# Optimization experiments

Measured on AMD Instinct MI355X. Metric: run time of the kernel, lower is better.

## Reference

```python
import jax, jax.numpy as jnp
import numpy as np
import math

N_HEAD = 16
D_MODEL = 1024
KSIZE = 3
PAD = 1


def _conv1d(x, w, b, pad):
    # x: [B, C_in, S], w: [C_out, C_in, K] (torch Conv1d layout)
    y = jax.lax.conv_general_dilated(
        x, w, window_strides=(1,), padding=[(pad, pad)],
        dimension_numbers=("NCH", "OIH", "NCH"))
    return y + b[None, :, None]


def setup_inputs() -> dict:
    key = jax.random.key(0)
    ks = jax.random.split(key, 10)
    B, S, D = 2, 2048, D_MODEL
    sc = 1.0 / math.sqrt(D)
    return {
        "q": jax.random.normal(ks[0], (B, S, D), jnp.float32),
        "k": jax.random.normal(ks[1], (B, S, D), jnp.float32),
        "v": jax.random.normal(ks[2], (B, S, D), jnp.float32),
        "wq_w": jax.random.normal(ks[3], (D, D, KSIZE), jnp.float32) * sc,
        "wq_b": jnp.zeros((D,), jnp.float32),
        "wk_w": jax.random.normal(ks[4], (D, D, KSIZE), jnp.float32) * sc,
        "wk_b": jnp.zeros((D,), jnp.float32),
        "wv_w": jax.random.normal(ks[5], (D, D, 1), jnp.float32) * sc,
        "wv_b": jnp.zeros((D,), jnp.float32),
        "wc_w": jax.random.normal(ks[6], (D, D), jnp.float32) * sc,
        "wc_b": jnp.zeros((D,), jnp.float32),
    }


def reference(q, k, v, wq_w, wq_b, wk_w, wk_b, wv_w, wv_b, wc_w, wc_b):
    B, S, D = q.shape
    h = N_HEAD
    d = D // h
    # channels-first for conv projections: [B, D, S]
    qc = _conv1d(jnp.swapaxes(q, 1, 2), wq_w, wq_b, PAD)
    kc = _conv1d(jnp.swapaxes(k, 1, 2), wk_w, wk_b, PAD)
    vc = _conv1d(jnp.swapaxes(v, 1, 2), wv_w, wv_b, 0)
    # faithful to torch: view(b, d, h, s) then transpose(1,2).transpose(2,3) -> [b, h, s, d]
    # (head index is the FAST axis of the channel dim, matching the original)
    qh = jnp.transpose(qc.reshape(B, d, h, S), (0, 2, 3, 1))
    kh = jnp.transpose(kc.reshape(B, d, h, S), (0, 2, 3, 1))
    vh = jnp.transpose(vc.reshape(B, d, h, S), (0, 2, 3, 1))
    scores = jnp.einsum("bhqd,bhkd->bhqk", qh, kh) / math.sqrt(d)
    attn = jax.nn.softmax(scores, axis=-1)
    out = jnp.einsum("bhqk,bhkd->bhqd", attn, vh)
    # concat: [b,h,s,d] -> [b,s,h*d]
    out = jnp.transpose(out, (0, 2, 1, 3)).reshape(B, S, D)
    # torch Linear: x @ W^T + b
    return out @ wc_w.T + wc_b
```

## Files before the change

### kernel.cpp

```cpp
#include <hip/hip_runtime.h>
#include <hip/hip_bf16.h>

#define SS 2048
#define DDIM 1024

typedef unsigned short u16;
typedef unsigned int u32;
typedef __attribute__((ext_vector_type(8))) short bf16x8_t;
typedef __attribute__((ext_vector_type(4))) float f32x4_t;

__device__ __forceinline__ u16 f2bf(float f) {
  __hip_bfloat16 h = __float2bfloat16(f);
  return *reinterpret_cast<u16*>(&h);
}

__device__ __forceinline__ void gld16(const void* g, void* lds_base) {
  __builtin_amdgcn_global_load_lds(
      (const __attribute__((address_space(1))) u32*)(uintptr_t)g,
      (__attribute__((address_space(3))) u32*)(u32)(uintptr_t)lds_base,
      16, 0, 0);
}

__global__ void zero_kernel(u32* zb) { zb[threadIdx.x] = 0u; }

__global__ __launch_bounds__(256) void convert3_kernel(
    const float* __restrict__ q, const float* __restrict__ k,
    const float* __restrict__ v, u16* __restrict__ Xq, u16* __restrict__ Xk,
    u16* __restrict__ Xv) {
  const int z = blockIdx.y;
  const float* src = (z == 0) ? q : (z == 1) ? k : v;
  u16* dst = (z == 0) ? Xq : (z == 1) ? Xk : Xv;
  int i = blockIdx.x * 256 + threadIdx.x;
  const float4* s = (const float4*)src + (size_t)i * 2;
  float4 f0 = s[0], f1 = s[1];
  u16 o[8] = {f2bf(f0.x), f2bf(f0.y), f2bf(f0.z), f2bf(f0.w),
              f2bf(f1.x), f2bf(f1.y), f2bf(f1.z), f2bf(f1.w)};
  *(uint4*)(dst + (size_t)i * 8) = *(const uint4*)o;
}

__global__ __launch_bounds__(256) void repack3_kernel(
    const float* __restrict__ wq, const float* __restrict__ wk,
    u16* __restrict__ Wqr, u16* __restrict__ Wkr) {
  const float* w = blockIdx.y ? wk : wq;
  u16* out = blockIdx.y ? Wkr : Wqr;
  int o = blockIdx.x;
  for (int j = threadIdx.x; j < 3072; j += 256) {
    int i = j / 3, t = j - i * 3;
    out[(size_t)o * 3072 + t * 1024 + i] = f2bf(w[(size_t)o * 3072 + j]);
  }
}

__global__ __launch_bounds__(256) void repackc_kernel(
    const float* __restrict__ wv, const float* __restrict__ wc,
    u16* __restrict__ Wvr, u16* __restrict__ Wcr) {
  const float* w = blockIdx.y ? wc : wv;
  u16* out = blockIdx.y ? Wcr : Wvr;
  size_t i = (size_t)blockIdx.x * 1024 + threadIdx.x * 4;
  float4 f = *(const float4*)(w + i);
  u16 o4[4] = {f2bf(f.x), f2bf(f.y), f2bf(f.z), f2bf(f.w)};
  *(ushort4*)(out + i) = *(const ushort4*)o4;
}

__global__ __launch_bounds__(256) void mfma_proj(
    const u16* __restrict__ Xq, const u16* __restrict__ Xk,
    const u16* __restrict__ Xv, const u16* __restrict__ Wq,
    const u16* __restrict__ Wk, const u16* __restrict__ Wv,
    const float* __restrict__ bq, const float* __restrict__ bk,
    const float* __restrict__ bv, u16* __restrict__ Qhb,
    u16* __restrict__ Khb, u16* __restrict__ Vtb,
    const u16* __restrict__ zbuf) {
  __shared__ __attribute__((aligned(16))) u16 As2[2][128][40];
  __shared__ __attribute__((aligned(16))) u16 Bs2[2][128][40];
  const int z = blockIdx.z;
  const u16* __restrict__ Xb = (z == 0) ? Xq : (z == 1) ? Xk : Xv;
  const u16* __restrict__ Wr = (z == 0) ? Wq : (z == 1) ? Wk : Wv;
  const float* __restrict__ bias = (z == 0) ? bq : (z == 1) ? bk : bv;
  u16* __restrict__ Cptr = (z == 0) ? Qhb : (z == 1) ? Khb : Vtb;
  const int nk = (z == 2) ? 32 : 96;
  const bool conv = (z < 2);
  const bool vout = (z == 2);
  const float scale = (z == 0) ? 0.125f : 1.0f;
  const int Kdim = (z == 2) ? 1024 : 3072;

  const int tid = threadIdx.x;
  const int lane = tid & 63;
  const int w = tid >> 6;
  const int ln = tid & 15;
  const int quad = (tid >> 4) & 3;
  const int wrow = w >> 1, wcol = w & 1;
  const int m0 = blockIdx.x * 128, n0 = blockIdx.y * 128;

  const char* p[5];
  int dinc[5];
  u32 ldso[5];
  bool act[5], isA[5], loA[5], hiA[5];
  const char* pbaseA[5];

#pragma unroll
  for (int i = 0; i < 5; ++i) {
    int c = w + 4 * i;
    isA[i] = (c < 10);
    if (c < 10) {
      int G = c * 64 + lane;
      int x = G / 5, kb = G - x * 5;
      int gm = m0 + x;
      int b = gm >> 11, s = gm & 2047;
      act[i] = (kb < 4);
      ldso[i] = c * 1024;
      const char* pb = (const char*)(Xb + (size_t)(b * SS + s) * DDIM + kb * 8);
      pbaseA[i] = pb;
      loA[i] = (s == 0);
      hiA[i] = (s == 2047);
      if (conv) {
        p[i] = loA[i] ? (const char*)zbuf : (pb - 2048);
        dinc[i] = loA[i] ? 0 : 64;
      } else {
        p[i] = pb;
        dinc[i] = 64;
      }
    } else {
      int c2 = c - 10;
      int G = c2 * 64 + lane;
      int x = G / 5, kb = G - x * 5;
      act[i] = (kb < 4);
      ldso[i] = c2 * 1024;
      p[i] = (const char*)(Wr + (size_t)(n0 + x) * Kdim + kb * 8);
      dinc[i] = 64;
      pbaseA[i] = nullptr;
      loA[i] = hiA[i] = false;
    }
  }

  auto stage = [&](int bi) {
#pragma unroll
    for (int i = 0; i < 5; ++i) {
      char* dst = (isA[i] ? (char*)As2[bi] : (char*)Bs2[bi]) + ldso[i];
      if (act[i]) gld16(p[i], dst);
      p[i] += dinc[i];
    }
  };

  f32x4_t acc[4][4];
#pragma unroll
  for (int i = 0; i < 4; ++i)
#pragma unroll
    for (int j = 0; j < 4; ++j) acc[i][j] = (f32x4_t){0.f, 0.f, 0.f, 0.f};

  stage(0);
  asm volatile("s_waitcnt vmcnt(0)" ::: "memory");
  __builtin_amdgcn_s_barrier();

#pragma unroll 2
  for (int ks = 0; ks < nk; ++ks) {
    const int cur = ks & 1;
    const int j = ks + 1;
    if (j < nk) {
      if (conv && (j & 31) == 0) {
#pragma unroll
        for (int i = 0; i < 5; ++i) {
          if (isA[i]) {
            if (j == 32) {
              if (loA[i]) { p[i] = pbaseA[i]; dinc[i] = 64; }
            } else {
              if (hiA[i]) { p[i] = (const char*)zbuf; dinc[i] = 0; }
            }
          }
        }
      }
      stage(cur ^ 1);
    }

    const u16(*As)[40] = As2[cur];
    const u16(*Bs)[40] = Bs2[cur];
    bf16x8_t a[4], b[4];
#pragma unroll
    for (int mt = 0; mt < 4; ++mt)
      a[mt] = *(const bf16x8_t*)&As[wrow * 64 + mt * 16 + ln][quad * 8];
#pragma unroll
    for (int nt = 0; nt < 4; ++nt)
      b[nt] = *(const bf16x8_t*)&Bs[wcol * 64 + nt * 16 + ln][quad * 8];
    __builtin_amdgcn_s_setprio(1);
#pragma unroll
    for (int mt = 0; mt < 4; ++mt)
#pragma unroll
      for (int nt = 0; nt < 4; ++nt)
        acc[mt][nt] = __builtin_amdgcn_mfma_f32_16x16x32_bf16(
            a[mt], b[nt], acc[mt][nt], 0, 0, 0);
    __builtin_amdgcn_s_setprio(0);

    asm volatile("s_waitcnt vmcnt(0) lgkmcnt(0)" ::: "memory");
    __builtin_amdgcn_s_barrier();
  }

#pragma unroll
  for (int mt = 0; mt < 4; ++mt) {
#pragma unroll
    for (int nt = 0; nt < 4; ++nt) {
      int gn = n0 + wcol * 64 + nt * 16 + ln;
      float bi = bias[gn];
#pragma unroll
      for (int r = 0; r < 4; ++r) {
        int gm = m0 + wrow * 64 + mt * 16 + quad * 4 + r;
        float val = (acc[mt][nt][r] + bi) * scale;
        int b = gm >> 11, s = gm & 2047;
        int hh = gn & 15, dd = gn >> 4;
        if (!vout)
          Cptr[((size_t)(b * 16 + hh) * SS + s) * 64 + dd] = f2bf(val);
        else
          Cptr[((size_t)(b * 16 + hh) * 64 + dd) * SS + s] = f2bf(val);
      }
    }
  }
}

__global__ __launch_bounds__(256) void mfma_gemm_lin(
    const u16* __restrict__ Xb, const u16* __restrict__ Wr,
    const float* __restrict__ bias, float* __restrict__ Cptr) {
  __shared__ __attribute__((aligned(16))) u16 As2[2][32][40];
  __shared__ __attribute__((aligned(16))) u16 Bs2[2][128][40];
  const int tid = threadIdx.x;
  const int lane = tid & 63;
  const int w = tid >> 6;
  const int ln = tid & 15;
  const int quad = (tid >> 4) & 3;
  const int wrow = w >> 1, wcol = w & 1;
  const int m0 = blockIdx.x * 32, n0 = blockIdx.y * 128;

  const char* p[4];
  u32 ldso[4];
  bool ok[4], act[4], isA[4];
#pragma unroll
  for (int i = 0; i < 4; ++i) {
    int c = w + 4 * i;
    ok[i] = (c < 13);
    if (c < 3) {
      int G = c * 64 + lane;
      int x = G / 5, kb = G - x * 5;
      isA[i] = true;
      act[i] = (kb < 4) && (x < 32);
      ldso[i] = c * 1024;
      p[i] = (const char*)(Xb + (size_t)(m0 + x) * DDIM + kb * 8);
    } else if (c < 13) {
      int c2 = c - 3;
      int G = c2 * 64 + lane;
      int x = G / 5, kb = G - x * 5;
      isA[i] = false;
      act[i] = (kb < 4);
      ldso[i] = c2 * 1024;
      p[i] = (const char*)(Wr + (size_t)(n0 + x) * 1024 + kb * 8);
    } else {
      isA[i] = false; act[i] = false; ldso[i] = 0; p[i] = nullptr;
    }
  }

  auto stage = [&](int bi) {
#pragma unroll
    for (int i = 0; i < 4; ++i) {
      if (ok[i]) {
        char* dst = (isA[i] ? (char*)As2[bi] : (char*)Bs2[bi]) + ldso[i];
        if (act[i]) gld16(p[i], dst);
        p[i] += 64;
      }
    }
  };

  f32x4_t acc[4];
#pragma unroll
  for (int j = 0; j < 4; ++j) acc[j] = (f32x4_t){0.f, 0.f, 0.f, 0.f};

  stage(0);
  asm volatile("s_waitcnt vmcnt(0)" ::: "memory");
  __builtin_amdgcn_s_barrier();

#pragma unroll 2
  for (int ks = 0; ks < 32; ++ks) {
    const int cur = ks & 1;
    if (ks + 1 < 32) stage(cur ^ 1);

    const u16(*As)[40] = As2[cur];
    const u16(*Bs)[40] = Bs2[cur];
    bf16x8_t a = *(const bf16x8_t*)&As[wrow * 16 + ln][quad * 8];
    bf16x8_t b[4];
#pragma unroll
    for (int nt = 0; nt < 4; ++nt)
      b[nt] = *(const bf16x8_t*)&Bs[wcol * 64 + nt * 16 + ln][quad * 8];
    __builtin_amdgcn_s_setprio(1);
#pragma unroll
    for (int nt = 0; nt < 4; ++nt)
      acc[nt] = __builtin_amdgcn_mfma_f32_16x16x32_bf16(a, b[nt], acc[nt], 0, 0, 0);
    __builtin_amdgcn_s_setprio(0);

    asm volatile("s_waitcnt vmcnt(0) lgkmcnt(0)" ::: "memory");
    __builtin_amdgcn_s_barrier();
  }

#pragma unroll
  for (int nt = 0; nt < 4; ++nt) {
    int gn = n0 + wcol * 64 + nt * 16 + ln;
    float bi = bias[gn];
#pragma unroll
    for (int r = 0; r < 4; ++r) {
      int gm = m0 + wrow * 16 + quad * 4 + r;
      Cptr[(size_t)gm * DDIM + gn] = acc[nt][r] + bi;
    }
  }
}

__global__ __launch_bounds__(256) void mfma_attn(
    const u16* __restrict__ Qhb, const u16* __restrict__ Khb,
    const u16* __restrict__ Vtb, u16* __restrict__ Aob,
    const u16* __restrict__ zbuf) {
  __shared__ __attribute__((aligned(16))) u16 Ks2[2][64][72];
  __shared__ __attribute__((aligned(16))) u16 Vt2[2][64][72];
  __shared__ __attribute__((aligned(16))) u16 Ps[4][16][72];
  const int tid = threadIdx.x;
  const int lane = tid & 63;
  const int w = tid >> 6;
  const int ln = tid & 15;
  const int quad = (tid >> 4) & 3;
  const int bh = blockIdx.y;
  const int b = bh >> 4, hh = bh & 15;
  const int s0 = blockIdx.x * 64;

  const char* p[5];
  int dinc[5];
  u32 ldso[5];
  bool ok[5], act[5], isK[5];
#pragma unroll
  for (int i = 0; i < 5; ++i) {
    int c = w + 4 * i;
    ok[i] = (c < 18);
    if (c < 9) {
      int G = c * 64 + lane;
      int x = G / 9, db = G - x * 9;
      isK[i] = true;
      act[i] = (db < 8);
      ldso[i] = c * 1024;
      p[i] = (const char*)(Khb + ((size_t)bh * SS + x) * 64 + db * 8);
      dinc[i] = 8192;
    } else if (c < 18) {
      int c2 = c - 9;
      int G = c2 * 64 + lane;
      int x = G / 9, db = G - x * 9;
      isK[i] = false;
      act[i] = (db < 8);
      ldso[i] = c2 * 1024;
      p[i] = (const char*)(Vtb + ((size_t)bh * 64 + x) * SS + db * 8);
      dinc[i] = 128;
    } else {
      isK[i] = false; ok[i] = false; act[i] = false; ldso[i] = 0;
      p[i] = nullptr; dinc[i] = 0;
    }
  }

  auto stage = [&](int bi) {
#pragma unroll
    for (int i = 0; i < 5; ++i) {
      if (ok[i]) {
        char* dst = (isK[i] ? (char*)Ks2[bi] : (char*)Vt2[bi]) + ldso[i];
        if (act[i]) gld16(p[i], dst);
        p[i] += dinc[i];
      }
    }
  };

  const u16* qp = Qhb + ((size_t)bh * SS + s0 + w * 16 + ln) * 64 + quad * 8;
  bf16x8_t qf0 = *(const bf16x8_t*)qp;
  bf16x8_t qf1 = *(const bf16x8_t*)(qp + 32);

  float mrow[4], lsum[4];
  f32x4_t oacc[4];
#pragma unroll
  for (int r = 0; r < 4; ++r) { mrow[r] = -3e38f; lsum[r] = 0.f; }
#pragma unroll
  for (int dt = 0; dt < 4; ++dt) oacc[dt] = (f32x4_t){0.f, 0.f, 0.f, 0.f};

  stage(0);
  asm volatile("s_waitcnt vmcnt(0)" ::: "memory");
  __builtin_amdgcn_s_barrier();

#pragma unroll 2
  for (int kt = 0; kt < 32; ++kt) {
    const int cur = kt & 1;
    if (kt + 1 < 32) stage(cur ^ 1);

    const u16(*Ks)[72] = Ks2[cur];
    const u16(*Vt)[72] = Vt2[cur];

    f32x4_t sc[4];
#pragma unroll
    for (int nt = 0; nt < 4; ++nt) sc[nt] = (f32x4_t){0.f, 0.f, 0.f, 0.f};
    __builtin_amdgcn_s_setprio(1);
#pragma unroll
    for (int nt = 0; nt < 4; ++nt) {
      bf16x8_t k0f = *(const bf16x8_t*)&Ks[nt * 16 + ln][quad * 8];
      sc[nt] = __builtin_amdgcn_mfma_f32_16x16x32_bf16(qf0, k0f, sc[nt], 0, 0, 0);
      bf16x8_t k1f = *(const bf16x8_t*)&Ks[nt * 16 + ln][32 + quad * 8];
      sc[nt] = __builtin_amdgcn_mfma_f32_16x16x32_bf16(qf1, k1f, sc[nt], 0, 0, 0);
    }
    __builtin_amdgcn_s_setprio(0);

    float mxv[4];
    bool need = false;
#pragma unroll
    for (int r = 0; r < 4; ++r) {
      float mx = fmaxf(fmaxf(sc[0][r], sc[1][r]), fmaxf(sc[2][r], sc[3][r]));
      mx = fmaxf(mx, __shfl_xor(mx, 1, 64));
      mx = fmaxf(mx, __shfl_xor(mx, 2, 64));
      mx = fmaxf(mx, __shfl_xor(mx, 4, 64));
      mx = fmaxf(mx, __shfl_xor(mx, 8, 64));
      mxv[r] = mx;
      need = need || (mx > mrow[r]);
    }
    if (__any(need)) {
#pragma unroll
      for (int r = 0; r < 4; ++r) {
        float mn = fmaxf(mrow[r], mxv[r]);
        float al = __expf(mrow[r] - mn);
        mrow[r] = mn;
        lsum[r] *= al;
#pragma unroll
        for (int dt = 0; dt < 4; ++dt) oacc[dt][r] *= al;
      }
    }
#pragma unroll
    for (int r = 0; r < 4; ++r) {
      float p0 = __expf(sc[0][r] - mrow[r]), p1 = __expf(sc[1][r] - mrow[r]);
      float p2 = __expf(sc[2][r] - mrow[r]), p3 = __expf(sc[3][r] - mrow[r]);
      lsum[r] += p0 + p1 + p2 + p3;
      Ps[w][quad * 4 + r][ln] = f2bf(p0);
      Ps[w][quad * 4 + r][16 + ln] = f2bf(p1);
      Ps[w][quad * 4 + r][32 + ln] = f2bf(p2);
      Ps[w][quad * 4 + r][48 + ln] = f2bf(p3);
    }

    bf16x8_t pa0 = *(const bf16x8_t*)&Ps[w][ln][quad * 8];
    bf16x8_t pa1 = *(const bf16x8_t*)&Ps[w][ln][32 + quad * 8];
    __builtin_amdgcn_s_setprio(1);
#pragma unroll
    for (int dt = 0; dt < 4; ++dt) {
      bf16x8_t v0f = *(const bf16x8_t*)&Vt[dt * 16 + ln][quad * 8];
      oacc[dt] = __builtin_amdgcn_mfma_f32_16x16x32_bf16(pa0, v0f, oacc[dt], 0, 0, 0);
      bf16x8_t v1f = *(const bf16x8_t*)&Vt[dt * 16 + ln][32 + quad * 8];
      oacc[dt] = __builtin_amdgcn_mfma_f32_16x16x32_bf16(pa1, v1f, oacc[dt], 0, 0, 0);
    }
    __builtin_amdgcn_s_setprio(0);

    asm volatile("s_waitcnt vmcnt(0) lgkmcnt(0)" ::: "memory");
    __builtin_amdgcn_s_barrier();
  }

  float inv[4];
#pragma unroll
  for (int r = 0; r < 4; ++r) {
    float t = lsum[r];
    t += __shfl_xor(t, 1, 64);
    t += __shfl_xor(t, 2, 64);
    t += __shfl_xor(t, 4, 64);
    t += __shfl_xor(t, 8, 64);
    inv[r] = 1.f / t;
  }
#pragma unroll
  for (int dt = 0; dt < 4; ++dt)
#pragma unroll
    for (int r = 0; r < 4; ++r) {
      int gm = b * SS + s0 + w * 16 + quad * 4 + r;
      Aob[(size_t)gm * DDIM + hh * 64 + dt * 16 + ln] = f2bf(oacc[dt][r] * inv[r]);
    }
}

extern "C" void kernel_launch(void* const* d_in, const int* in_sizes, int n_in,
                              void* d_out, int out_size, void* d_ws, size_t ws_size,
                              hipStream_t stream) {
  const float* q    = (const float*)d_in[0];
  const float* k    = (const float*)d_in[1];
  const float* v    = (const float*)d_in[2];
  const float* wq_w = (const float*)d_in[3];
  const float* wq_b = (const float*)d_in[4];
  const float* wk_w = (const float*)d_in[5];
  const float* wk_b = (const float*)d_in[6];
  const float* wv_w = (const float*)d_in[7];
  const float* wv_b = (const float*)d_in[8];
  const float* wc_w = (const float*)d_in[9];
  const float* wc_b = (const float*)d_in[10];

  char* ws = (char*)d_ws;
  size_t off = 0;
  u16* zbuf = (u16*)(ws + off); off += 256;
  const size_t SZ_ACT = (size_t)2 * SS * DDIM * 2;
  u16* Xq  = (u16*)(ws + off); off += SZ_ACT;
  u16* Xk  = (u16*)(ws + off); off += SZ_ACT;
  u16* Xv  = (u16*)(ws + off); off += SZ_ACT;
  u16* Wqr = (u16*)(ws + off); off += (size_t)1024 * 3072 * 2;
  u16* Wkr = (u16*)(ws + off); off += (size_t)1024 * 3072 * 2;
  u16* Wvr = (u16*)(ws + off); off += (size_t)1024 * 1024 * 2;
  u16* Wcr = (u16*)(ws + off); off += (size_t)1024 * 1024 * 2;
  u16* Qhb = (u16*)(ws + off); off += SZ_ACT;
  u16* Khb = (u16*)(ws + off); off += SZ_ACT;
  u16* Vtb = (u16*)(ws + off); off += SZ_ACT;
  u16* Aob = (u16*)(ws + off); off += SZ_ACT;
  if (ws_size < off) return;

  zero_kernel<<<1, 64, 0, stream>>>((u32*)zbuf);
  convert3_kernel<<<dim3(2048, 3), 256, 0, stream>>>(q, k, v, Xq, Xk, Xv);
  repack3_kernel<<<dim3(1024, 2), 256, 0, stream>>>(wq_w, wk_w, Wqr, Wkr);
  repackc_kernel<<<dim3(1024, 2), 256, 0, stream>>>(wv_w, wc_w, Wvr, Wcr);

  mfma_proj<<<dim3(32, 8, 3), 256, 0, stream>>>(
      Xq, Xk, Xv, Wqr, Wkr, Wvr, wq_b, wk_b, wv_b, Qhb, Khb, Vtb, zbuf);

  mfma_attn<<<dim3(32, 32), 256, 0, stream>>>(Qhb, Khb, Vtb, Aob, zbuf);

  mfma_gemm_lin<<<dim3(128, 8), 256, 0, stream>>>(Aob, Wcr, wc_b, (float*)d_out);
}
```

Measured before the change: 394.9 us.

## Prefetch two tiles ahead with partial vmcnt waits in GEMM and attention loops

Result: no change. 393.1 us (-0.5%).

```diff
diff --git a/kernel.cpp b/kernel.cpp
--- a/kernel.cpp
+++ b/kernel.cpp
@@ -147,13 +147,28 @@
     for (int j = 0; j < 4; ++j) acc[i][j] = (f32x4_t){0.f, 0.f, 0.f, 0.f};
 
   stage(0);
-  asm volatile("s_waitcnt vmcnt(0)" ::: "memory");
-  __builtin_amdgcn_s_barrier();
+  stage(1);
 
 #pragma unroll 2
   for (int ks = 0; ks < nk; ++ks) {
     const int cur = ks & 1;
-    const int j = ks + 1;
+    if (ks + 1 < nk)
+      asm volatile("s_waitcnt vmcnt(5)\ns_barrier" ::: "memory");
+    else
+      asm volatile("s_waitcnt vmcnt(0)\ns_barrier" ::: "memory");
+
+    const u16(*As)[40] = As2[cur];
+    const u16(*Bs)[40] = Bs2[cur];
+    bf16x8_t a[4], b[4];
+#pragma unroll
+    for (int mt = 0; mt < 4; ++mt)
+      a[mt] = *(const bf16x8_t*)&As[wrow * 64 + mt * 16 + ln][quad * 8];
+#pragma unroll
+    for (int nt = 0; nt < 4; ++nt)
+      b[nt] = *(const bf16x8_t*)&Bs[wcol * 64 + nt * 16 + ln][quad * 8];
+    asm volatile("s_waitcnt lgkmcnt(0)\ns_barrier" ::: "memory");
+
+    const int j = ks + 2;
     if (j < nk) {
       if (conv && (j & 31) == 0) {
 #pragma unroll
@@ -167,18 +182,9 @@
           }
         }
       }
-      stage(cur ^ 1);
-    }
-
-    const u16(*As)[40] = As2[cur];
-    const u16(*Bs)[40] = Bs2[cur];
-    bf16x8_t a[4], b[4];
-#pragma unroll
-    for (int mt = 0; mt < 4; ++mt)
-      a[mt] = *(const bf16x8_t*)&As[wrow * 64 + mt * 16 + ln][quad * 8];
-#pragma unroll
-    for (int nt = 0; nt < 4; ++nt)
-      b[nt] = *(const bf16x8_t*)&Bs[wcol * 64 + nt * 16 + ln][quad * 8];
+      stage(cur);
+    }
+
     __builtin_amdgcn_s_setprio(1);
 #pragma unroll
     for (int mt = 0; mt < 4; ++mt)
@@ -187,9 +193,6 @@
         acc[mt][nt] = __builtin_amdgcn_mfma_f32_16x16x32_bf16(
             a[mt], b[nt], acc[mt][nt], 0, 0, 0);
     __builtin_amdgcn_s_setprio(0);
-
-    asm volatile("s_waitcnt vmcnt(0) lgkmcnt(0)" ::: "memory");
-    __builtin_amdgcn_s_barrier();
   }
 
 #pragma unroll
@@ -269,13 +272,17 @@
   for (int j = 0; j < 4; ++j) acc[j] = (f32x4_t){0.f, 0.f, 0.f, 0.f};
 
   stage(0);
-  asm volatile("s_waitcnt vmcnt(0)" ::: "memory");
-  __builtin_amdgcn_s_barrier();
+  stage(1);
 
 #pragma unroll 2
   for (int ks = 0; ks < 32; ++ks) {
     const int cur = ks & 1;
-    if (ks + 1 < 32) stage(cur ^ 1);
+    if (ks + 1 < 32) {
+      if (w == 0) asm volatile("s_waitcnt vmcnt(4)\ns_barrier" ::: "memory");
+      else        asm volatile("s_waitcnt vmcnt(3)\ns_barrier" ::: "memory");
+    } else {
+      asm volatile("s_waitcnt vmcnt(0)\ns_barrier" ::: "memory");
+    }
 
     const u16(*As)[40] = As2[cur];
     const u16(*Bs)[40] = Bs2[cur];
@@ -284,14 +291,15 @@
 #pragma unroll
     for (int nt = 0; nt < 4; ++nt)
       b[nt] = *(const bf16x8_t*)&Bs[wcol * 64 + nt * 16 + ln][quad * 8];
+    asm volatile("s_waitcnt lgkmcnt(0)\ns_barrier" ::: "memory");
+
+    if (ks + 2 < 32) stage(cur);
+
     __builtin_amdgcn_s_setprio(1);
 #pragma unroll
     for (int nt = 0; nt < 4; ++nt)
       acc[nt] = __builtin_amdgcn_mfma_f32_16x16x32_bf16(a, b[nt], acc[nt], 0, 0, 0);
     __builtin_amdgcn_s_setprio(0);
-
-    asm volatile("s_waitcnt vmcnt(0) lgkmcnt(0)" ::: "memory");
-    __builtin_amdgcn_s_barrier();
   }
 
 #pragma unroll
@@ -376,13 +384,17 @@
   for (int dt = 0; dt < 4; ++dt) oacc[dt] = (f32x4_t){0.f, 0.f, 0.f, 0.f};
 
   stage(0);
-  asm volatile("s_waitcnt vmcnt(0)" ::: "memory");
-  __builtin_amdgcn_s_barrier();
+  stage(1);
 
 #pragma unroll 2
   for (int kt = 0; kt < 32; ++kt) {
     const int cur = kt & 1;
-    if (kt + 1 < 32) stage(cur ^ 1);
+    if (kt + 1 < 32) {
+      if (w < 2) asm volatile("s_waitcnt vmcnt(5)\ns_barrier" ::: "memory");
+      else       asm volatile("s_waitcnt vmcnt(4)\ns_barrier" ::: "memory");
+    } else {
+      asm volatile("s_waitcnt vmcnt(0)\ns_barrier" ::: "memory");
+    }
 
     const u16(*Ks)[72] = Ks2[cur];
     const u16(*Vt)[72] = Vt2[cur];
@@ -446,8 +458,8 @@
     }
     __builtin_amdgcn_s_setprio(0);
 
-    asm volatile("s_waitcnt vmcnt(0) lgkmcnt(0)" ::: "memory");
-    __builtin_amdgcn_s_barrier();
+    asm volatile("s_waitcnt lgkmcnt(0)\ns_barrier" ::: "memory");
+    if (kt + 2 < 32) stage(cur);
   }
 
   float inv[4];
```
